# Kernel tuning notes

Hardware: AMD Instinct MI355X
Metric: run time of the kernel (lower is better)

The kernel has to match this reference:

```python
import jax, jax.numpy as jnp
import numpy as np

D_MODEL = 1024
NUM_HEADS = 16
HEAD_DIM = D_MODEL // NUM_HEADS
THETA = 10000.0
B, S = 2, 2048


def setup_inputs() -> dict:
    key = jax.random.key(0)
    ks = jax.random.split(key, 9)
    std = 1.0 / np.sqrt(D_MODEL)
    x = jax.random.normal(ks[0], (B, S, D_MODEL), dtype=jnp.float32)
    Wq = jax.random.normal(ks[1], (D_MODEL, D_MODEL), dtype=jnp.float32) * std
    Wk = jax.random.normal(ks[2], (D_MODEL, D_MODEL), dtype=jnp.float32) * std
    Wv = jax.random.normal(ks[3], (D_MODEL, D_MODEL), dtype=jnp.float32) * std
    Wo = jax.random.normal(ks[4], (D_MODEL, D_MODEL), dtype=jnp.float32) * std
    bq = jax.random.normal(ks[5], (D_MODEL,), dtype=jnp.float32) * std
    bk = jax.random.normal(ks[6], (D_MODEL,), dtype=jnp.float32) * std
    bv = jax.random.normal(ks[7], (D_MODEL,), dtype=jnp.float32) * std
    bo = jax.random.normal(ks[8], (D_MODEL,), dtype=jnp.float32) * std
    return {"x": x, "Wq": Wq, "bq": bq, "Wk": Wk, "bk": bk,
            "Wv": Wv, "bv": bv, "Wo": Wo, "bo": bo}


def _apply_rope(t, cos, sin):
    # t: [B, H, S, hd]; cos/sin: [S, hd//2]; interleaved-pair rotation
    t1 = t[..., 0::2]
    t2 = t[..., 1::2]
    r1 = t1 * cos - t2 * sin
    r2 = t1 * sin + t2 * cos
    return jnp.stack([r1, r2], axis=-1).reshape(t.shape)


def reference(x, Wq, bq, Wk, bk, Wv, bv, Wo, bo):
    B_, S_, D = x.shape
    H, hd = NUM_HEADS, HEAD_DIM
    # QKV projections (nn.Linear: x @ W.T + b)
    q = (x @ Wq.T + bq).reshape(B_, S_, H, hd).transpose(0, 2, 1, 3)  # [B,H,S,hd]
    k = (x @ Wk.T + bk).reshape(B_, S_, H, hd).transpose(0, 2, 1, 3)
    v = (x @ Wv.T + bv).reshape(B_, S_, H, hd).transpose(0, 2, 1, 3)
    # RoPE with token_positions = arange(S)
    pos = jnp.arange(S_, dtype=jnp.float32)
    inv_freq = 1.0 / (THETA ** (jnp.arange(0, hd, 2, dtype=jnp.float32) / hd))
    ang = pos[:, None] * inv_freq[None, :]  # [S, hd//2]
    cos, sin = jnp.cos(ang), jnp.sin(ang)
    q = _apply_rope(q, cos, sin)
    k = _apply_rope(k, cos, sin)
    # causal scaled-dot-product attention
    scores = jnp.einsum('bhqd,bhkd->bhqk', q, k) / jnp.sqrt(jnp.asarray(hd, x.dtype))
    causal = jnp.arange(S_)[:, None] >= jnp.arange(S_)[None, :]  # [S,S]
    scores = jnp.where(causal, scores, -jnp.inf)
    attn = jax.nn.softmax(scores, axis=-1)
    out = jnp.einsum('bhqk,bhkd->bhqd', attn, v)  # [B,H,S,hd]
    out = out.transpose(0, 2, 1, 3).reshape(B_, S_, D)
    return out @ Wo.T + bo
```

## Files before the change

### kernel.cpp

```cpp
#include <hip/hip_runtime.h>
#include <hip/hip_bf16.h>
#include <stdint.h>

typedef __bf16 bf16_t;
typedef __bf16 bf16x4 __attribute__((ext_vector_type(4)));
typedef __bf16 bf16x8 __attribute__((ext_vector_type(8)));
typedef float  f32x4  __attribute__((ext_vector_type(4)));

#define DM    1024
#define NH    16
#define HD    64
#define SEQ   2048
#define BATCH 2
#define BS    (BATCH*SEQ)
#define NQKV  (3*DM)

#define GLOAD_LDS16(g, l) \
  __builtin_amdgcn_global_load_lds((const __attribute__((address_space(1))) void*)(g), \
                                   (__attribute__((address_space(3))) void*)(l), 16, 0, 0)

__device__ __forceinline__ f32x4 mfma16(bf16x8 a, bf16x8 b, f32x4 c) {
  return __builtin_amdgcn_mfma_f32_16x16x32_bf16(a, b, c, 0, 0, 0);
}

__global__ __launch_bounds__(256) void k_cast_all(
    const float* __restrict__ x,  const float* __restrict__ Wq,
    const float* __restrict__ Wk, const float* __restrict__ Wv,
    const float* __restrict__ Wo, const float* __restrict__ bq,
    const float* __restrict__ bk, const float* __restrict__ bv,
    bf16_t* __restrict__ xb, bf16_t* __restrict__ Wcat,
    bf16_t* __restrict__ Wob, float* __restrict__ bcat,
    float2* __restrict__ rt)
{
  const int bid = blockIdx.x, tid = threadIdx.x;
  if (bid >= 4099) {
    const int idx = (bid - 4099) * 256 + tid;
    const int s = idx >> 5, i = idx & 31;
    float inv = powf(10000.0f, -(float)(2 * i) / 64.0f);
    float ang = (float)s * inv;
    rt[idx] = make_float2(cosf(ang), sinf(ang));
    return;
  }
  if (bid >= 4096) {
    const int k = bid - 4096;
    const float* src = (k == 0) ? bq : (k == 1) ? bk : bv;
    *(float4*)&bcat[k * DM + tid * 4] = *(const float4*)&src[tid * 4];
    return;
  }
  const float* src; bf16_t* dst; int i;
  if (bid < 2048)      { src = x;  dst = xb;                i = bid * 2048 + tid * 8; }
  else if (bid < 2560) { src = Wq; dst = Wcat;              i = (bid - 2048) * 2048 + tid * 8; }
  else if (bid < 3072) { src = Wk; dst = Wcat + DM * DM;    i = (bid - 2560) * 2048 + tid * 8; }
  else if (bid < 3584) { src = Wv; dst = Wcat + 2 * DM * DM;i = (bid - 3072) * 2048 + tid * 8; }
  else                 { src = Wo; dst = Wob;               i = (bid - 3584) * 2048 + tid * 8; }
  float4 a = *(const float4*)(src + i);
  float4 b = *(const float4*)(src + i + 4);
  bf16x8 o;
  o[0] = (bf16_t)a.x; o[1] = (bf16_t)a.y; o[2] = (bf16_t)a.z; o[3] = (bf16_t)a.w;
  o[4] = (bf16_t)b.x; o[5] = (bf16_t)b.y; o[6] = (bf16_t)b.z; o[7] = (bf16_t)b.w;
  *(bf16x8*)(dst + i) = o;
}

__global__ __launch_bounds__(256) void k_gemm_qk(
    const bf16_t* __restrict__ A, const bf16_t* __restrict__ B,
    const float* __restrict__ bias, const float2* __restrict__ rt,
    bf16_t* __restrict__ Qo, bf16_t* __restrict__ Ko)
{
  const int K = DM;
  __shared__ __align__(16) bf16_t As[2][128 * 32];
  __shared__ __align__(16) bf16_t Bs[2][128 * 32];
  const int tid  = threadIdx.x;
  const int lane = tid & 63;
  const int wave = tid >> 6;
  const int wr = wave >> 1, wc = wave & 1;
  const int m0 = blockIdx.y * 128, n0 = blockIdx.x * 128;
  const int c16 = lane & 15, g = lane >> 4;

  f32x4 acc[4][4];
  #pragma unroll
  for (int i = 0; i < 4; ++i)
    #pragma unroll
    for (int j = 0; j < 4; ++j)
      #pragma unroll
      for (int e = 0; e < 4; ++e) acc[i][j][e] = 0.0f;

  const int srow = wave * 32;
  const int lrow = lane >> 2;
  const int lk   = (lane & 3) * 8;
  const bf16_t* ga0 = A + (size_t)(m0 + srow +      lrow) * K + lk;
  const bf16_t* ga1 = A + (size_t)(m0 + srow + 16 + lrow) * K + lk;
  const bf16_t* gb0 = B + (size_t)(n0 + srow +      lrow) * K + lk;
  const bf16_t* gb1 = B + (size_t)(n0 + srow + 16 + lrow) * K + lk;
  bf16_t* la0A = &As[0][(srow) * 32];      bf16_t* la0B = &As[1][(srow) * 32];
  bf16_t* la1A = &As[0][(srow + 16) * 32]; bf16_t* la1B = &As[1][(srow + 16) * 32];
  bf16_t* lb0A = &Bs[0][(srow) * 32];      bf16_t* lb0B = &Bs[1][(srow) * 32];
  bf16_t* lb1A = &Bs[0][(srow + 16) * 32]; bf16_t* lb1B = &Bs[1][(srow + 16) * 32];

  const int po = (wr * 64 + c16) * 32 + g * 8;
  const int qo = (wc * 64 + c16) * 32 + g * 8;
  const bf16_t* paA = &As[0][po]; const bf16_t* paB = &As[1][po];
  const bf16_t* pbA = &Bs[0][qo]; const bf16_t* pbB = &Bs[1][qo];

  GLOAD_LDS16(ga0, la0A); GLOAD_LDS16(ga1, la1A);
  GLOAD_LDS16(gb0, lb0A); GLOAD_LDS16(gb1, lb1A);
  __syncthreads();

  for (int it = 0; it < K / 32; ++it) {
    const bool odd = it & 1;
    const int kt = it * 32;
    if (kt + 32 < K) {
      GLOAD_LDS16(ga0 + kt + 32, odd ? la0A : la0B);
      GLOAD_LDS16(ga1 + kt + 32, odd ? la1A : la1B);
      GLOAD_LDS16(gb0 + kt + 32, odd ? lb0A : lb0B);
      GLOAD_LDS16(gb1 + kt + 32, odd ? lb1A : lb1B);
    }
    const bf16_t* pa = odd ? paB : paA;
    const bf16_t* pb = odd ? pbB : pbA;
    bf16x8 af[4], bfr[4];
    #pragma unroll
    for (int t = 0; t < 4; ++t) af[t]  = *(const bf16x8*)(pa + t * 16 * 32);
    #pragma unroll
    for (int t = 0; t < 4; ++t) bfr[t] = *(const bf16x8*)(pb + t * 16 * 32);
    #pragma unroll
    for (int i = 0; i < 4; ++i)
      #pragma unroll
      for (int j = 0; j < 4; ++j)
        acc[i][j] = mfma16(bfr[j], af[i], acc[i][j]);
    __syncthreads();
  }

  const int region = n0 >> 10;
  bf16_t* dst = region ? Ko : Qo;
  const float qs = region ? 1.0f : (0.125f * 1.44269504088896f);
  #pragma unroll
  for (int j = 0; j < 4; ++j) {
    const int nb = n0 + wc * 64 + j * 16 + (g << 2);
    const float4 bv = *(const float4*)&bias[nb];
    const int h  = (nb >> 6) & 15;
    const int d0 = nb & 63;
    #pragma unroll
    for (int i = 0; i < 4; ++i) {
      const int m = m0 + wr * 64 + i * 16 + c16;
      const int s = m & 2047;
      const int bh = ((m >> 11) << 4) + h;
      const float4 cs = *(const float4*)&rt[(size_t)s * 32 + (d0 >> 1)];
      const float v0 = acc[i][j][0] + bv.x;
      const float v1 = acc[i][j][1] + bv.y;
      const float v2 = acc[i][j][2] + bv.z;
      const float v3 = acc[i][j][3] + bv.w;
      bf16x4 ov;
      ov[0] = (bf16_t)((v0 * cs.x - v1 * cs.y) * qs);
      ov[1] = (bf16_t)((v0 * cs.y + v1 * cs.x) * qs);
      ov[2] = (bf16_t)((v2 * cs.z - v3 * cs.w) * qs);
      ov[3] = (bf16_t)((v2 * cs.w + v3 * cs.z) * qs);
      *(bf16x4*)&dst[((size_t)bh * SEQ + s) * HD + d0] = ov;
    }
  }
}

__global__ __launch_bounds__(256) void k_gemm_v(
    const bf16_t* __restrict__ A, const bf16_t* __restrict__ B,
    const float* __restrict__ bias, bf16_t* __restrict__ Vt)
{
  const int K = DM;
  __shared__ __align__(16) bf16_t As[2][128 * 32];
  __shared__ __align__(16) bf16_t Bs[2][128 * 32];
  const int tid  = threadIdx.x;
  const int lane = tid & 63;
  const int wave = tid >> 6;
  const int wr = wave >> 1, wc = wave & 1;
  const int m0 = blockIdx.y * 128, n0 = blockIdx.x * 128;
  const int c16 = lane & 15, g = lane >> 4;

  f32x4 acc[4][4];
  #pragma unroll
  for (int i = 0; i < 4; ++i)
    #pragma unroll
    for (int j = 0; j < 4; ++j)
      #pragma unroll
      for (int e = 0; e < 4; ++e) acc[i][j][e] = 0.0f;

  const int srow = wave * 32;
  const int lrow = lane >> 2;
  const int lk   = (lane & 3) * 8;
  const bf16_t* ga0 = A + (size_t)(m0 + srow +      lrow) * K + lk;
  const bf16_t* ga1 = A + (size_t)(m0 + srow + 16 + lrow) * K + lk;
  const bf16_t* gb0 = B + (size_t)(n0 + srow +      lrow) * K + lk;
  const bf16_t* gb1 = B + (size_t)(n0 + srow + 16 + lrow) * K + lk;
  bf16_t* la0A = &As[0][(srow) * 32];      bf16_t* la0B = &As[1][(srow) * 32];
  bf16_t* la1A = &As[0][(srow + 16) * 32]; bf16_t* la1B = &As[1][(srow + 16) * 32];
  bf16_t* lb0A = &Bs[0][(srow) * 32];      bf16_t* lb0B = &Bs[1][(srow) * 32];
  bf16_t* lb1A = &Bs[0][(srow + 16) * 32]; bf16_t* lb1B = &Bs[1][(srow + 16) * 32];

  const int po = (wr * 64 + c16) * 32 + g * 8;
  const int qo = (wc * 64 + c16) * 32 + g * 8;
  const bf16_t* paA = &As[0][po]; const bf16_t* paB = &As[1][po];
  const bf16_t* pbA = &Bs[0][qo]; const bf16_t* pbB = &Bs[1][qo];

  GLOAD_LDS16(ga0, la0A); GLOAD_LDS16(ga1, la1A);
  GLOAD_LDS16(gb0, lb0A); GLOAD_LDS16(gb1, lb1A);
  __syncthreads();

  for (int it = 0; it < K / 32; ++it) {
    const bool odd = it & 1;
    const int kt = it * 32;
    if (kt + 32 < K) {
      GLOAD_LDS16(ga0 + kt + 32, odd ? la0A : la0B);
      GLOAD_LDS16(ga1 + kt + 32, odd ? la1A : la1B);
      GLOAD_LDS16(gb0 + kt + 32, odd ? lb0A : lb0B);
      GLOAD_LDS16(gb1 + kt + 32, odd ? lb1A : lb1B);
    }
    const bf16_t* pa = odd ? paB : paA;
    const bf16_t* pb = odd ? pbB : pbA;
    bf16x8 af[4], bfr[4];
    #pragma unroll
    for (int t = 0; t < 4; ++t) af[t]  = *(const bf16x8*)(pa + t * 16 * 32);
    #pragma unroll
    for (int t = 0; t < 4; ++t) bfr[t] = *(const bf16x8*)(pb + t * 16 * 32);
    #pragma unroll
    for (int i = 0; i < 4; ++i)
      #pragma unroll
      for (int j = 0; j < 4; ++j)
        acc[i][j] = mfma16(af[i], bfr[j], acc[i][j]);
    __syncthreads();
  }

  const int rbase = m0 + wr * 64 + (g << 2);
  const int cbase = n0 + wc * 64 + c16;
  #pragma unroll
  for (int j = 0; j < 4; ++j) {
    const int c = cbase + j * 16;
    const float bv = bias[c];
    const int h = (c >> 6) & 15;
    const int d = c & 63;
    #pragma unroll
    for (int i = 0; i < 4; ++i) {
      bf16x4 ov;
      #pragma unroll
      for (int e = 0; e < 4; ++e) ov[e] = (bf16_t)(acc[i][j][e] + bv);
      const int r0 = rbase + i * 16;
      const int bh = ((r0 >> 11) << 4) + h;
      const int s0 = r0 & 2047;
      const int u  = (s0 >> 4) & 3;
      const int p0 = (s0 & ~63) + ((u >> 1) << 5) + (g << 3) + ((u & 1) << 2);
      *(bf16x4*)&Vt[((size_t)bh * HD + d) * SEQ + p0] = ov;
    }
  }
}

__global__ __launch_bounds__(512) void k_gemm_out(
    const bf16_t* __restrict__ A, const bf16_t* __restrict__ B,
    const float* __restrict__ bias, float* __restrict__ C)
{
  const int K = DM, N = DM;
  __shared__ __align__(16) bf16_t As[2][128 * 32];
  __shared__ __align__(16) bf16_t Bs[2][128 * 32];
  const int tid  = threadIdx.x;
  const int lane = tid & 63;
  const int w    = tid >> 6;
  const int wr = w >> 2, wc = w & 3;
  const int m0 = blockIdx.y * 128, n0 = blockIdx.x * 128;
  const int c16 = lane & 15, g = lane >> 4;

  f32x4 acc[4][2];
  #pragma unroll
  for (int i = 0; i < 4; ++i)
    #pragma unroll
    for (int j = 0; j < 2; ++j)
      #pragma unroll
      for (int e = 0; e < 4; ++e) acc[i][j][e] = 0.0f;

  const int lrow = lane >> 2;
  const int lk   = (lane & 3) * 8;
  const bf16_t* ga = A + (size_t)(m0 + w * 16 + lrow) * K + lk;
  const bf16_t* gb = B + (size_t)(n0 + w * 16 + lrow) * K + lk;
  bf16_t* laA = &As[0][(w * 16) * 32]; bf16_t* laB = &As[1][(w * 16) * 32];
  bf16_t* lbA = &Bs[0][(w * 16) * 32]; bf16_t* lbB = &Bs[1][(w * 16) * 32];

  const int po = (wr * 64 + c16) * 32 + g * 8;
  const int qo = (wc * 32 + c16) * 32 + g * 8;
  const bf16_t* paA = &As[0][po]; const bf16_t* paB = &As[1][po];
  const bf16_t* pbA = &Bs[0][qo]; const bf16_t* pbB = &Bs[1][qo];

  GLOAD_LDS16(ga, laA); GLOAD_LDS16(gb, lbA);
  __syncthreads();

  for (int it = 0; it < K / 32; ++it) {
    const bool odd = it & 1;
    const int kt = it * 32;
    if (kt + 32 < K) {
      GLOAD_LDS16(ga + kt + 32, odd ? laA : laB);
      GLOAD_LDS16(gb + kt + 32, odd ? lbA : lbB);
    }
    const bf16_t* pa = odd ? paB : paA;
    const bf16_t* pb = odd ? pbB : pbA;
    bf16x8 af[4], bfr[2];
    #pragma unroll
    for (int t = 0; t < 4; ++t) af[t]  = *(const bf16x8*)(pa + t * 16 * 32);
    #pragma unroll
    for (int t = 0; t < 2; ++t) bfr[t] = *(const bf16x8*)(pb + t * 16 * 32);
    #pragma unroll
    for (int i = 0; i < 4; ++i)
      #pragma unroll
      for (int j = 0; j < 2; ++j)
        acc[i][j] = mfma16(af[i], bfr[j], acc[i][j]);
    __syncthreads();
  }

  const int rbase = m0 + wr * 64 + (g << 2);
  const int cbase = n0 + wc * 32 + c16;
  #pragma unroll
  for (int j = 0; j < 2; ++j) {
    const int c = cbase + j * 16;
    const float bv = bias[c];
    #pragma unroll
    for (int i = 0; i < 4; ++i) {
      #pragma unroll
      for (int e = 0; e < 4; ++e) {
        const int r = rbase + i * 16 + e;
        C[(size_t)r * N + c] = acc[i][j][e] + bv;
      }
    }
  }
}

__global__ __launch_bounds__(256, 2) void k_attn(
    const bf16_t* __restrict__ Q, const bf16_t* __restrict__ K,
    const bf16_t* __restrict__ Vt, bf16_t* __restrict__ O)
{
  __shared__ __align__(16) bf16_t kbuf[2][64 * 64];
  __shared__ __align__(16) bf16_t vbuf[2][64 * 64];
  const int tid = threadIdx.x, lane = tid & 63, w = tid >> 6;
  const int pr = blockIdx.x >> 5;
  const int bh = blockIdx.x & 31;
  const int b  = bh >> 4, h = bh & 15;
  const int c16 = lane & 15;
  const int g   = lane >> 4;

  const bf16_t* Qb = Q  + (size_t)bh * SEQ * HD;
  const bf16_t* Kb = K  + (size_t)bh * SEQ * HD;
  const bf16_t* Vb = Vt + (size_t)bh * HD * SEQ;

  const int qtA = pr, qtB = 31 - pr;
  const int qA  = qtA * 64 + w * 16 + c16;
  const int qB  = qtB * 64 + w * 16 + c16;
  const int Tmax = qtB + 1;

  bf16x8 qfA0 = *(const bf16x8*)&Qb[(size_t)qA * HD + g * 8];
  bf16x8 qfA1 = *(const bf16x8*)&Qb[(size_t)qA * HD + 32 + g * 8];
  bf16x8 qfB0 = *(const bf16x8*)&Qb[(size_t)qB * HD + g * 8];
  bf16x8 qfB1 = *(const bf16x8*)&Qb[(size_t)qB * HD + 32 + g * 8];

  f32x4 oaccA[4], oaccB[4];
  #pragma unroll
  for (int dblk = 0; dblk < 4; ++dblk)
    #pragma unroll
    for (int e = 0; e < 4; ++e) { oaccA[dblk][e] = 0.0f; oaccB[dblk][e] = 0.0f; }
  float mA = -1e30f, lA = 0.0f, mB = -1e30f, lB = 0.0f;

  const int soff0 = w * 1024 + lane * 16;
  const int soff1 = soff0 + 4096;
  const int srow0 = soff0 >> 7, srow1 = soff1 >> 7;
  const int scb0  = (soff0 & 127) ^ ((srow0 & 7) << 4);
  const int scb1  = (soff1 & 127) ^ ((srow1 & 7) << 4);
  const bf16_t* gk0 = &Kb[(size_t)srow0 * HD + (scb0 >> 1)];
  const bf16_t* gk1 = &Kb[(size_t)srow1 * HD + (scb1 >> 1)];
  const bf16_t* gv0 = &Vb[(size_t)srow0 * SEQ + (scb0 >> 1)];
  const bf16_t* gv1 = &Vb[(size_t)srow1 * SEQ + (scb1 >> 1)];
  bf16_t* lk0A = &kbuf[0][(w * 1024) >> 1];
  bf16_t* lk1A = &kbuf[0][(w * 1024 + 4096) >> 1];
  bf16_t* lk0B = &kbuf[1][(w * 1024) >> 1];
  bf16_t* lk1B = &kbuf[1][(w * 1024 + 4096) >> 1];
  bf16_t* lv0A = &vbuf[0][(w * 1024) >> 1];
  bf16_t* lv1A = &vbuf[0][(w * 1024 + 4096) >> 1];
  bf16_t* lv0B = &vbuf[1][(w * 1024) >> 1];
  bf16_t* lv1B = &vbuf[1][(w * 1024 + 4096) >> 1];

  const int sw = (c16 & 7) << 4;
  const int e0 = ((16 * g) ^ sw) >> 1;
  const int dhi = (((64 + 16 * g) ^ sw) >> 1) - e0;
  const bf16_t* kp0 = &kbuf[0][c16 * 64 + e0];
  const bf16_t* kp1 = &kbuf[1][c16 * 64 + e0];
  const bf16_t* vp0 = &vbuf[0][c16 * 64 + e0];
  const bf16_t* vp1 = &vbuf[1][c16 * 64 + e0];

  GLOAD_LDS16(gk0, lk0A); GLOAD_LDS16(gk1, lk1A);
  GLOAD_LDS16(gv0, lv0A); GLOAD_LDS16(gv1, lv1A);
  gk0 += 4096; gk1 += 4096; gv0 += 64; gv1 += 64;
  __syncthreads();

  for (int t = 0; t < Tmax; ++t) {
    const bool odd = t & 1;
    if (t + 1 < Tmax) {
      GLOAD_LDS16(gk0, odd ? lk0A : lk0B); GLOAD_LDS16(gk1, odd ? lk1A : lk1B);
      GLOAD_LDS16(gv0, odd ? lv0A : lv0B); GLOAD_LDS16(gv1, odd ? lv1A : lv1B);
      gk0 += 4096; gk1 += 4096; gv0 += 64; gv1 += 64;
    }

    const bf16_t* kp = odd ? kp1 : kp0;
    const bf16_t* vp = odd ? vp1 : vp0;

    bf16x8 kf0[4], kf1[4], vlo[4], vhi[4];
    #pragma unroll
    for (int u = 0; u < 4; ++u) {
      kf0[u] = *(const bf16x8*)(kp + u * 1024);
      kf1[u] = *(const bf16x8*)(kp + u * 1024 + dhi);
    }
    #pragma unroll
    for (int dblk = 0; dblk < 4; ++dblk) {
      vlo[dblk] = *(const bf16x8*)(vp + dblk * 1024);
      vhi[dblk] = *(const bf16x8*)(vp + dblk * 1024 + dhi);
    }

    {
      f32x4 st[4];
      __builtin_amdgcn_s_setprio(1);
      #pragma unroll
      for (int u = 0; u < 4; ++u) {
        f32x4 z; z[0] = z[1] = z[2] = z[3] = 0.0f;
        z = mfma16(kf0[u], qfB0, z);
        z = mfma16(kf1[u], qfB1, z);
        st[u] = z;
      }
      __builtin_amdgcn_s_setprio(0);

      float pv[16];
      if (t == qtB) {
        const int kv0 = t * 64;
        #pragma unroll
        for (int u = 0; u < 4; ++u)
          #pragma unroll
          for (int r = 0; r < 4; ++r) {
            const int kv = kv0 + 16 * u + 4 * g + r;
            pv[u * 4 + r] = (kv <= qB) ? st[u][r] : -1e30f;
          }
      } else {
        #pragma unroll
        for (int u = 0; u < 4; ++u)
          #pragma unroll
          for (int r = 0; r < 4; ++r)
            pv[u * 4 + r] = st[u][r];
      }

      float ma = fmaxf(fmaxf(pv[0], pv[1]), fmaxf(pv[2], pv[3]));
      float mb = fmaxf(fmaxf(pv[4], pv[5]), fmaxf(pv[6], pv[7]));
      float mc = fmaxf(fmaxf(pv[8], pv[9]), fmaxf(pv[10], pv[11]));
      float md = fmaxf(fmaxf(pv[12], pv[13]), fmaxf(pv[14], pv[15]));
      const float lmx = fmaxf(fmaxf(ma, mb), fmaxf(mc, md));

      if (__any(lmx - mB > 12.0f)) {
        float mx = fmaxf(lmx, __shfl_xor(lmx, 16));
        mx = fmaxf(mx, __shfl_xor(mx, 32));
        const float mn = fmaxf(mB, mx);
        const float alpha = exp2f(mB - mn);
        lB *= alpha;
        #pragma unroll
        for (int dblk = 0; dblk < 4; ++dblk)
          #pragma unroll
          for (int e = 0; e < 4; ++e) oaccB[dblk][e] *= alpha;
        mB = mn;
      }

      #pragma unroll
      for (int i = 0; i < 16; ++i) pv[i] = exp2f(pv[i] - mB);
      float s0 = (pv[0] + pv[1]) + (pv[2] + pv[3]);
      float s1 = (pv[4] + pv[5]) + (pv[6] + pv[7]);
      float s2 = (pv[8] + pv[9]) + (pv[10] + pv[11]);
      float s3 = (pv[12] + pv[13]) + (pv[14] + pv[15]);
      lB += (s0 + s1) + (s2 + s3);

      bf16x8 pf0, pf1;
      #pragma unroll
      for (int j = 0; j < 8; ++j) {
        pf0[j] = (bf16_t)pv[j];
        pf1[j] = (bf16_t)pv[8 + j];
      }

      __builtin_amdgcn_s_setprio(1);
      #pragma unroll
      for (int dblk = 0; dblk < 4; ++dblk) {
        oaccB[dblk] = mfma16(vlo[dblk], pf0, oaccB[dblk]);
        oaccB[dblk] = mfma16(vhi[dblk], pf1, oaccB[dblk]);
      }
      __builtin_amdgcn_s_setprio(0);
    }

    if (t <= qtA) {
      f32x4 st[4];
      __builtin_amdgcn_s_setprio(1);
      #pragma unroll
      for (int u = 0; u < 4; ++u) {
        f32x4 z; z[0] = z[1] = z[2] = z[3] = 0.0f;
        z = mfma16(kf0[u], qfA0, z);
        z = mfma16(kf1[u], qfA1, z);
        st[u] = z;
      }
      __builtin_amdgcn_s_setprio(0);

      float pv[16];
      if (t == qtA) {
        const int kv0 = t * 64;
        #pragma unroll
        for (int u = 0; u < 4; ++u)
          #pragma unroll
          for (int r = 0; r < 4; ++r) {
            const int kv = kv0 + 16 * u + 4 * g + r;
            pv[u * 4 + r] = (kv <= qA) ? st[u][r] : -1e30f;
          }
      } else {
        #pragma unroll
        for (int u = 0; u < 4; ++u)
          #pragma unroll
          for (int r = 0; r < 4; ++r)
            pv[u * 4 + r] = st[u][r];
      }

      float ma = fmaxf(fmaxf(pv[0], pv[1]), fmaxf(pv[2], pv[3]));
      float mb = fmaxf(fmaxf(pv[4], pv[5]), fmaxf(pv[6], pv[7]));
      float mc = fmaxf(fmaxf(pv[8], pv[9]), fmaxf(pv[10], pv[11]));
      float md = fmaxf(fmaxf(pv[12], pv[13]), fmaxf(pv[14], pv[15]));
      const float lmx = fmaxf(fmaxf(ma, mb), fmaxf(mc, md));

      if (__any(lmx - mA > 12.0f)) {
        float mx = fmaxf(lmx, __shfl_xor(lmx, 16));
        mx = fmaxf(mx, __shfl_xor(mx, 32));
        const float mn = fmaxf(mA, mx);
        const float alpha = exp2f(mA - mn);
        lA *= alpha;
        #pragma unroll
        for (int dblk = 0; dblk < 4; ++dblk)
          #pragma unroll
          for (int e = 0; e < 4; ++e) oaccA[dblk][e] *= alpha;
        mA = mn;
      }

      #pragma unroll
      for (int i = 0; i < 16; ++i) pv[i] = exp2f(pv[i] - mA);
      float s0 = (pv[0] + pv[1]) + (pv[2] + pv[3]);
      float s1 = (pv[4] + pv[5]) + (pv[6] + pv[7]);
      float s2 = (pv[8] + pv[9]) + (pv[10] + pv[11]);
      float s3 = (pv[12] + pv[13]) + (pv[14] + pv[15]);
      lA += (s0 + s1) + (s2 + s3);

      bf16x8 pf0, pf1;
      #pragma unroll
      for (int j = 0; j < 8; ++j) {
        pf0[j] = (bf16_t)pv[j];
        pf1[j] = (bf16_t)pv[8 + j];
      }

      __builtin_amdgcn_s_setprio(1);
      #pragma unroll
      for (int dblk = 0; dblk < 4; ++dblk) {
        oaccA[dblk] = mfma16(vlo[dblk], pf0, oaccA[dblk]);
        oaccA[dblk] = mfma16(vhi[dblk], pf1, oaccA[dblk]);
      }
      __builtin_amdgcn_s_setprio(0);
    }

    __syncthreads();
  }

  lA += __shfl_xor(lA, 16);
  lA += __shfl_xor(lA, 32);
  lB += __shfl_xor(lB, 16);
  lB += __shfl_xor(lB, 32);
  const float invA = 1.0f / lA;
  const float invB = 1.0f / lB;
  bf16_t* orowA = O + ((size_t)(b * SEQ + qA)) * DM + h * HD;
  bf16_t* orowB = O + ((size_t)(b * SEQ + qB)) * DM + h * HD;
  #pragma unroll
  for (int dblk = 0; dblk < 4; ++dblk) {
    bf16x4 ovA, ovB;
    #pragma unroll
    for (int r = 0; r < 4; ++r) {
      ovA[r] = (bf16_t)(oaccA[dblk][r] * invA);
      ovB[r] = (bf16_t)(oaccB[dblk][r] * invB);
    }
    *(bf16x4*)&orowA[dblk * 16 + 4 * g] = ovA;
    *(bf16x4*)&orowB[dblk * 16 + 4 * g] = ovB;
  }
}

extern "C" void kernel_launch(void* const* d_in, const int* in_sizes, int n_in,
                              void* d_out, int out_size, void* d_ws, size_t ws_size,
                              hipStream_t stream)
{
  const float* x  = (const float*)d_in[0];
  const float* Wq = (const float*)d_in[1];
  const float* bq = (const float*)d_in[2];
  const float* Wk = (const float*)d_in[3];
  const float* bk = (const float*)d_in[4];
  const float* Wv = (const float*)d_in[5];
  const float* bv = (const float*)d_in[6];
  const float* Wo = (const float*)d_in[7];
  const float* bo = (const float*)d_in[8];
  float* out = (float*)d_out;

  char* ws = (char*)d_ws;
  size_t off = 0;
  auto alloc = [&](size_t bytes) { char* p = ws + off; off += (bytes + 255) & ~255ULL; return p; };
  bf16_t* xb   = (bf16_t*)alloc((size_t)BS * DM * 2);
  bf16_t* Wcat = (bf16_t*)alloc((size_t)NQKV * DM * 2);
  bf16_t* Wob  = (bf16_t*)alloc((size_t)DM * DM * 2);
  float*  bcat = (float*)alloc((size_t)NQKV * 4);
  float2* rt   = (float2*)alloc((size_t)SEQ * 32 * 8);
  bf16_t* Qh   = (bf16_t*)alloc((size_t)BS * DM * 2);
  bf16_t* Kh   = (bf16_t*)alloc((size_t)BS * DM * 2);
  bf16_t* Vth  = (bf16_t*)alloc((size_t)BS * DM * 2);
  bf16_t* Oh   = (bf16_t*)alloc((size_t)BS * DM * 2);
  (void)ws_size; (void)in_sizes; (void)n_in; (void)out_size;

  k_cast_all<<<4099 + 256, 256, 0, stream>>>(x, Wq, Wk, Wv, Wo, bq, bk, bv,
                                             xb, Wcat, Wob, bcat, rt);

  dim3 gqk(16, 32);
  k_gemm_qk<<<gqk, 256, 0, stream>>>(xb, Wcat, bcat, rt, Qh, Kh);
  dim3 gv(8, 32);
  k_gemm_v<<<gv, 256, 0, stream>>>(xb, Wcat + 2 * DM * DM, bcat + 2 * DM, Vth);
  k_attn<<<512, 256, 0, stream>>>(Qh, Kh, Vth, Oh);
  dim3 g2(DM / 128, BS / 128);
  k_gemm_out<<<g2, 512, 0, stream>>>(Oh, Wob, bo, out);
}
```

Baseline: 121.2 us.

## Stage K/V tiles in pairs with four LDS buffers, one barrier per two tiles

Attention LDS staging grows from double to quadruple buffering. Two KV tiles are prefetched per group and both are computed before a single __syncthreads, which halves the number of barriers and gives loads more time in flight. This doubles LDS use to 64KB per block, which may cut occupancy below the launch-bounds target of 2 blocks per CU.

```diff
diff --git a/kernel.cpp b/kernel.cpp
--- a/kernel.cpp
+++ b/kernel.cpp
@@ -328,8 +328,8 @@
     const bf16_t* __restrict__ Q, const bf16_t* __restrict__ K,
     const bf16_t* __restrict__ Vt, bf16_t* __restrict__ O)
 {
-  __shared__ __align__(16) bf16_t kbuf[2][64 * 64];
-  __shared__ __align__(16) bf16_t vbuf[2][64 * 64];
+  __shared__ __align__(16) bf16_t kls[4 * 4096];
+  __shared__ __align__(16) bf16_t vls[4 * 4096];
   const int tid = threadIdx.x, lane = tid & 63, w = tid >> 6;
   const int pr = blockIdx.x >> 5;
   const int bh = blockIdx.x & 31;
@@ -367,38 +367,28 @@
   const bf16_t* gk1 = &Kb[(size_t)srow1 * HD + (scb1 >> 1)];
   const bf16_t* gv0 = &Vb[(size_t)srow0 * SEQ + (scb0 >> 1)];
   const bf16_t* gv1 = &Vb[(size_t)srow1 * SEQ + (scb1 >> 1)];
-  bf16_t* lk0A = &kbuf[0][(w * 1024) >> 1];
-  bf16_t* lk1A = &kbuf[0][(w * 1024 + 4096) >> 1];
-  bf16_t* lk0B = &kbuf[1][(w * 1024) >> 1];
-  bf16_t* lk1B = &kbuf[1][(w * 1024 + 4096) >> 1];
-  bf16_t* lv0A = &vbuf[0][(w * 1024) >> 1];
-  bf16_t* lv1A = &vbuf[0][(w * 1024 + 4096) >> 1];
-  bf16_t* lv0B = &vbuf[1][(w * 1024) >> 1];
-  bf16_t* lv1B = &vbuf[1][(w * 1024 + 4096) >> 1];
+  const int wd0 = (w * 1024) >> 1;
+  const int wd1 = wd0 + 2048;
 
   const int sw = (c16 & 7) << 4;
   const int e0 = ((16 * g) ^ sw) >> 1;
   const int dhi = (((64 + 16 * g) ^ sw) >> 1) - e0;
-  const bf16_t* kp0 = &kbuf[0][c16 * 64 + e0];
-  const bf16_t* kp1 = &kbuf[1][c16 * 64 + e0];
-  const bf16_t* vp0 = &vbuf[0][c16 * 64 + e0];
-  const bf16_t* vp1 = &vbuf[1][c16 * 64 + e0];
-
-  GLOAD_LDS16(gk0, lk0A); GLOAD_LDS16(gk1, lk1A);
-  GLOAD_LDS16(gv0, lv0A); GLOAD_LDS16(gv1, lv1A);
-  gk0 += 4096; gk1 += 4096; gv0 += 64; gv1 += 64;
-  __syncthreads();
-
-  for (int t = 0; t < Tmax; ++t) {
-    const bool odd = t & 1;
-    if (t + 1 < Tmax) {
-      GLOAD_LDS16(gk0, odd ? lk0A : lk0B); GLOAD_LDS16(gk1, odd ? lk1A : lk1B);
-      GLOAD_LDS16(gv0, odd ? lv0A : lv0B); GLOAD_LDS16(gv1, odd ? lv1A : lv1B);
-      gk0 += 4096; gk1 += 4096; gv0 += 64; gv1 += 64;
-    }
-
-    const bf16_t* kp = odd ? kp1 : kp0;
-    const bf16_t* vp = odd ? vp1 : vp0;
+  const int fro = c16 * 64 + e0;
+
+  auto STAGE = [&](int tt) {
+    const int slot = (((tt >> 1) & 1) << 1) | (tt & 1);
+    const size_t gko = (size_t)tt * 4096;
+    const size_t gvo = (size_t)tt * 64;
+    GLOAD_LDS16(gk0 + gko, kls + slot * 4096 + wd0);
+    GLOAD_LDS16(gk1 + gko, kls + slot * 4096 + wd1);
+    GLOAD_LDS16(gv0 + gvo, vls + slot * 4096 + wd0);
+    GLOAD_LDS16(gv1 + gvo, vls + slot * 4096 + wd1);
+  };
+
+  auto COMPUTE = [&](int tt) {
+    const int slot = (((tt >> 1) & 1) << 1) | (tt & 1);
+    const bf16_t* kp = kls + slot * 4096 + fro;
+    const bf16_t* vp = vls + slot * 4096 + fro;
 
     bf16x8 kf0[4], kf1[4], vlo[4], vhi[4];
     #pragma unroll
@@ -425,8 +415,8 @@
       __builtin_amdgcn_s_setprio(0);
 
       float pv[16];
-      if (t == qtB) {
-        const int kv0 = t * 64;
+      if (tt == qtB) {
+        const int kv0 = tt * 64;
         #pragma unroll
         for (int u = 0; u < 4; ++u)
           #pragma unroll
@@ -485,7 +475,7 @@
       __builtin_amdgcn_s_setprio(0);
     }
 
-    if (t <= qtA) {
+    if (tt <= qtA) {
       f32x4 st[4];
       __builtin_amdgcn_s_setprio(1);
       #pragma unroll
@@ -498,8 +488,8 @@
       __builtin_amdgcn_s_setprio(0);
 
       float pv[16];
-      if (t == qtA) {
-        const int kv0 = t * 64;
+      if (tt == qtA) {
+        const int kv0 = tt * 64;
         #pragma unroll
         for (int u = 0; u < 4; ++u)
           #pragma unroll
@@ -557,7 +547,19 @@
       }
       __builtin_amdgcn_s_setprio(0);
     }
-
+  };
+
+  STAGE(0);
+  if (1 < Tmax) STAGE(1);
+  __syncthreads();
+
+  const int ngrp = (Tmax + 1) >> 1;
+  for (int gp = 0; gp < ngrp; ++gp) {
+    const int t0 = 2 * gp;
+    if (t0 + 2 < Tmax) STAGE(t0 + 2);
+    if (t0 + 3 < Tmax) STAGE(t0 + 3);
+    COMPUTE(t0);
+    if (t0 + 1 < Tmax) COMPUTE(t0 + 1);
     __syncthreads();
   }
 
```

New measurement: 123.7 us. +2.0%, slower.
